# Kernel optimization log

Measured on AMD Instinct MI355X. Metric: run time of the kernel, lower is better.

## Reference

```python
import jax, jax.numpy as jnp
import numpy as np

BITW = 1
BITA = 3
BATCH = 8192
IN_CH = 4096
N_UNITS = 4096


def _quantize(x, k):
    # DoReFa uniform quantizer with straight-through estimator (round -> identity grad)
    n = float(2 ** k - 1)
    return x + jax.lax.stop_gradient(jnp.round(x * n) / n - x)


def _cabs(x):
    # clip magnitude to [0, 1]
    return jnp.minimum(1.0, jnp.abs(x))


def quantize_active(x, bitA):
    if bitA == 32:
        return x
    return _quantize(x, bitA)


def quantize_weight(w, bitW):
    if bitW == 32:
        return w
    if bitW == 1:
        # binary weights scaled by mean |w| (E is treated as constant)
        E = jax.lax.stop_gradient(jnp.mean(jnp.abs(w)))
        y = w / E
        # sign with straight-through gradient
        return (y + jax.lax.stop_gradient(jnp.sign(y) - y)) * E
    t = jnp.tanh(w)
    t = t / jnp.max(jnp.abs(t)) * 0.5 + 0.5
    return 2.0 * _quantize(t, bitW) - 1.0


def setup_inputs() -> dict:
    key = jax.random.key(0)
    k1, k2 = jax.random.split(key)
    inputs = jax.random.normal(k1, (BATCH, IN_CH), dtype=jnp.float32)
    # truncated_normal(stddev=0.1) init approximated with normal * 0.1
    W = jax.random.normal(k2, (IN_CH, N_UNITS), dtype=jnp.float32) * 0.1
    b = jnp.zeros((N_UNITS,), dtype=jnp.float32)
    return {"inputs": inputs, "W": W, "b": b}


def reference(inputs, W, b):
    q_in = quantize_active(_cabs(inputs), BITA)   # [B, IN] in {0..1} grid of 2^bitA-1 levels
    q_W = quantize_weight(W, BITW)                # [IN, OUT] binary (+-E)
    out = jnp.matmul(q_in, q_W) + b               # [B, OUT]
    return out
```

## Files before the change

### kernel.cpp

```cpp
#include <hip/hip_runtime.h>


static constexpr int BATCH  = 8192;
static constexpr int IN_CH  = 4096;
static constexpr int NUNITS = 4096;
static constexpr int TPB    = 256;

typedef int v4i __attribute__((ext_vector_type(4)));

static constexpr size_t A8_OFF   = 0;
static constexpr size_t A8_BYTES = (size_t)BATCH * IN_CH;
static constexpr size_t BT_OFF   = A8_OFF + A8_BYTES;
static constexpr size_t BT_BYTES = (size_t)NUNITS * IN_CH;
static constexpr int    NPART    = 4096;
static constexpr size_t PART_OFF = BT_OFF + BT_BYTES;
static constexpr size_t SCALE_OFF= PART_OFF + NPART * sizeof(float);

__global__ __launch_bounds__(TPB) void k_signT(const float* __restrict__ W,
                                               char* __restrict__ bt,
                                               float* __restrict__ partials) {
    __shared__ char tile[64][68];
    __shared__ float red[TPB];
    const int bk = blockIdx.x & 63;
    const int bn = blockIdx.x >> 6;
    const int t  = threadIdx.x;
    const int c4 = (t & 15) * 4;
    const int r0 = t >> 4;
    float asum = 0.f;
#pragma unroll
    for (int i = 0; i < 4; ++i) {
        const int r = i * 16 + r0;
        float4 w = *(const float4*)(W + (size_t)(bk * 64 + r) * NUNITS + bn * 64 + c4);
        asum += fabsf(w.x) + fabsf(w.y) + fabsf(w.z) + fabsf(w.w);
        tile[c4 + 0][r] = (w.x > 0.f) ? 1 : ((w.x < 0.f) ? -1 : 0);
        tile[c4 + 1][r] = (w.y > 0.f) ? 1 : ((w.y < 0.f) ? -1 : 0);
        tile[c4 + 2][r] = (w.z > 0.f) ? 1 : ((w.z < 0.f) ? -1 : 0);
        tile[c4 + 3][r] = (w.w > 0.f) ? 1 : ((w.w < 0.f) ? -1 : 0);
    }
    __syncthreads();
    const int n  = t >> 2;
    const int kk = (t & 3) * 16;
    char o[16];
#pragma unroll
    for (int j = 0; j < 16; ++j) o[j] = tile[n][kk + j];
    *(uint4*)(bt + (size_t)(bn * 64 + n) * IN_CH + bk * 64 + kk) = *(const uint4*)o;

    red[t] = asum;
    __syncthreads();
    for (int off = TPB / 2; off > 0; off >>= 1) {
        if (t < off) red[t] += red[t + off];
        __syncthreads();
    }
    if (t == 0) partials[blockIdx.x] = red[0];
}

__device__ __forceinline__ unsigned int q4(float4 v) {
    unsigned int b0 = (unsigned int)(int)rintf(fminf(1.0f, fabsf(v.x)) * 7.0f);
    unsigned int b1 = (unsigned int)(int)rintf(fminf(1.0f, fabsf(v.y)) * 7.0f);
    unsigned int b2 = (unsigned int)(int)rintf(fminf(1.0f, fabsf(v.z)) * 7.0f);
    unsigned int b3 = (unsigned int)(int)rintf(fminf(1.0f, fabsf(v.w)) * 7.0f);
    return b0 | (b1 << 8) | (b2 << 16) | (b3 << 24);
}

__global__ __launch_bounds__(TPB) void k_quant_a(const float4* __restrict__ x4,
                                                 uint4* __restrict__ a16,
                                                 const float* __restrict__ partials,
                                                 float* __restrict__ scale) {
    if (blockIdx.x == 0) {
        __shared__ float red[TPB];
        float s = 0.f;
        for (int i = threadIdx.x; i < NPART; i += TPB) s += partials[i];
        red[threadIdx.x] = s;
        __syncthreads();
        for (int off = TPB / 2; off > 0; off >>= 1) {
            if ((int)threadIdx.x < off) red[threadIdx.x] += red[threadIdx.x + off];
            __syncthreads();
        }
        if (threadIdx.x == 0) {
            float E = red[0] / (float)((size_t)IN_CH * NUNITS);
            *scale = E / 7.0f;
        }
    }
    const size_t t = (size_t)blockIdx.x * TPB + threadIdx.x;
    uint4 o;
    o.x = q4(x4[t * 4 + 0]);
    o.y = q4(x4[t * 4 + 1]);
    o.z = q4(x4[t * 4 + 2]);
    o.w = q4(x4[t * 4 + 3]);
    a16[t] = o;
}

__device__ __forceinline__ void gload_lds16(const void* g, void* l) {
    __builtin_amdgcn_global_load_lds((const __attribute__((address_space(1))) void*)g,
                                     (__attribute__((address_space(3))) void*)l,
                                     16, 0, 0);
}

#define VMCNT0   asm volatile("s_waitcnt vmcnt(0)" ::: "memory")
#define LGKM0    asm volatile("s_waitcnt lgkmcnt(0)" ::: "memory")
#define SCHEDB   __builtin_amdgcn_sched_barrier(0)
#define BARRIER  __builtin_amdgcn_s_barrier()
#define PRIO1    __builtin_amdgcn_s_setprio(1)
#define PRIO0    __builtin_amdgcn_s_setprio(0)

static constexpr int NI = IN_CH / 128;

__global__ __launch_bounds__(1024, 4) void k_gemm(const char* __restrict__ A8,
                                                  const char* __restrict__ BT,
                                                  const float* __restrict__ scale_p,
                                                  const float* __restrict__ bias,
                                                  float* __restrict__ out) {
    __shared__ char Ms[2][65536];

    const int t    = threadIdx.x;
    const int bid  = blockIdx.x;
    const int swzb = (bid & 7) * 64 + (bid >> 3);
    const int bRow = swzb >> 4;
    const int bCol = swzb & 15;
    const int lane = t & 63;
    const int wid  = t >> 6;
    const int wr   = wid >> 2;
    const int wc   = wid & 3;
    const int lr   = lane & 15;
    const int lk4  = lane >> 4;

    const int aoff = ((lk4 ^ (lr & 7)) << 4);
    const int boff = aoff ^ 64;

    const int lslot = (t & 7) ^ ((t >> 3) & 7);
    const char* mbase = (lslot < 4)
        ? (A8 + (size_t)(bRow * 256) * IN_CH)
        : (BT + (size_t)(bCol * 256) * IN_CH);
    const char* sbase = mbase + (size_t)(t >> 3) * IN_CH + ((lslot & 3) << 4);

    v4i acc[4][4] = {};

#define STAGE4(P, STG)                                                           \
    _Pragma("unroll") for (int c = 0; c < 2; ++c)                                \
        _Pragma("unroll") for (int h = 0; h < 2; ++h)                            \
            gload_lds16(sbase + (size_t)h * 128 * IN_CH + ((size_t)(P) * 128 + c * 64), \
                        (STG) + c * 32768 + h * 16384 + t * 16)

#define CHUNK(CUR, c)                                                            \
    do {                                                                         \
        const char* _cp = (CUR) + (c) * 32768;                                   \
        v4i a_[4], b_[4];                                                        \
        _Pragma("unroll") for (int m = 0; m < 4; ++m)                            \
            a_[m] = *(const v4i*)(_cp + (wr * 64 + m * 16 + lr) * 128 + aoff);   \
        _Pragma("unroll") for (int n = 0; n < 4; ++n)                            \
            b_[n] = *(const v4i*)(_cp + (wc * 64 + n * 16 + lr) * 128 + boff);   \
        PRIO1;                                                                   \
        _Pragma("unroll") for (int m = 0; m < 4; ++m)                            \
            _Pragma("unroll") for (int n = 0; n < 4; ++n)                        \
                acc[m][n] = __builtin_amdgcn_mfma_i32_16x16x64_i8(               \
                    a_[m], b_[n], acc[m][n], 0, 0, 0);                           \
        PRIO0;                                                                   \
    } while (0)

#define INTERVAL(P, CUR, STG, DOSTG)                                             \
    do {                                                                         \
        SCHEDB; LGKM0;                                                           \
        VMCNT0;                                                                  \
        BARRIER; SCHEDB;                                                         \
        if (DOSTG) { STAGE4((P) + 1, STG); }                                     \
        CHUNK(CUR, 0);                                                           \
        CHUNK(CUR, 1);                                                           \
    } while (0)

    char* B0 = (char*)Ms[0];
    char* B1 = (char*)Ms[1];

    STAGE4(0, B0);

    for (int P = 0; P < NI - 2; P += 2) {
        INTERVAL(P,     B0, B1, 1);
        INTERVAL(P + 1, B1, B0, 1);
    }
    INTERVAL(NI - 2, B0, B1, 1);
    INTERVAL(NI - 1, B1, B0, 0);

    const float scale = *scale_p;
    const int orow0 = bRow * 256 + wr * 64;
    const int ocol0 = bCol * 256 + wc * 64;
#pragma unroll
    for (int m = 0; m < 4; ++m) {
#pragma unroll
        for (int n = 0; n < 4; ++n) {
            const int col = ocol0 + n * 16 + lr;
            const float bb = bias[col];
            const int rbase = orow0 + m * 16 + lk4 * 4;
#pragma unroll
            for (int j = 0; j < 4; ++j)
                out[(size_t)(rbase + j) * NUNITS + col] = scale * (float)acc[m][n][j] + bb;
        }
    }
#undef STAGE4
#undef CHUNK
#undef INTERVAL
}

extern "C" void kernel_launch(void* const* d_in, const int* in_sizes, int n_in,
                              void* d_out, int out_size, void* d_ws, size_t ws_size,
                              hipStream_t stream) {
    const float* x  = (const float*)d_in[0];
    const float* W  = (const float*)d_in[1];
    const float* b  = (const float*)d_in[2];
    float* out      = (float*)d_out;

    char*  ws       = (char*)d_ws;
    char*  A8       = ws + A8_OFF;
    char*  BT       = ws + BT_OFF;
    float* partials = (float*)(ws + PART_OFF);
    float* scale    = (float*)(ws + SCALE_OFF);

    k_signT<<<(IN_CH / 64) * (NUNITS / 64), TPB, 0, stream>>>(W, BT, partials);
    k_quant_a<<<(BATCH * (IN_CH / 16)) / TPB, TPB, 0, stream>>>((const float4*)x, (uint4*)A8,
                                                                partials, scale);
    k_gemm<<<(BATCH / 256) * (NUNITS / 256), 1024, 0, stream>>>(A8, BT, scale, b, out);
}
```

Measured before the change: 167.6 us.

## Pack binary weights to 2 bits in MFMA fragment order and expand in-register

The sign kernel now writes weight signs as 2-bit codes packed into dwords, laid out in the exact per-lane fragment order the GEMM consumes. The GEMM stages only a quarter of the previous B bytes into LDS and expands each packed dword to int8 fragments with v_perm lookups before the MFMAs. The A tile layout and swizzle are reorganised to match the smaller LDS footprint. This cuts global and LDS traffic for B, but adds VALU permute work inside the MFMA loop, and the B staging now uses 4-byte direct-to-LDS loads.

Result: slower. 248.1 us (+48.0%).

```diff
diff --git a/kernel.cpp b/kernel.cpp
--- a/kernel.cpp
+++ b/kernel.cpp
@@ -10,14 +10,14 @@
 
 static constexpr size_t A8_OFF   = 0;
 static constexpr size_t A8_BYTES = (size_t)BATCH * IN_CH;
-static constexpr size_t BT_OFF   = A8_OFF + A8_BYTES;
-static constexpr size_t BT_BYTES = (size_t)NUNITS * IN_CH;
+static constexpr size_t PB_OFF   = A8_OFF + A8_BYTES;
+static constexpr size_t PB_BYTES = (size_t)NUNITS * IN_CH / 4;
 static constexpr int    NPART    = 4096;
-static constexpr size_t PART_OFF = BT_OFF + BT_BYTES;
+static constexpr size_t PART_OFF = PB_OFF + PB_BYTES;
 static constexpr size_t SCALE_OFF= PART_OFF + NPART * sizeof(float);
 
 __global__ __launch_bounds__(TPB) void k_signT(const float* __restrict__ W,
-                                               char* __restrict__ bt,
+                                               unsigned int* __restrict__ pb,
                                                float* __restrict__ partials) {
     __shared__ char tile[64][68];
     __shared__ float red[TPB];
@@ -38,12 +38,16 @@
         tile[c4 + 3][r] = (w.w > 0.f) ? 1 : ((w.w < 0.f) ? -1 : 0);
     }
     __syncthreads();
-    const int n  = t >> 2;
-    const int kk = (t & 3) * 16;
-    char o[16];
-#pragma unroll
-    for (int j = 0; j < 16; ++j) o[j] = tile[n][kk + j];
-    *(uint4*)(bt + (size_t)(bn * 64 + n) * IN_CH + bk * 64 + kk) = *(const uint4*)o;
+    const int cl   = t & 63;
+    const int lk4p = t >> 6;
+    unsigned int d = 0;
+#pragma unroll
+    for (int j = 0; j < 16; ++j)
+        d |= ((unsigned int)(unsigned char)tile[cl][lk4p * 16 + j] & 3u) << (2 * j);
+    const int lanep = lk4p * 16 + (cl & 15);
+    const size_t dw = (size_t)(bn >> 2) * 65536 + (size_t)bk * 1024
+                    + (size_t)(bn & 3) * 256 + lanep * 4 + (cl >> 4);
+    pb[dw] = d;
 
     red[t] = asum;
     __syncthreads();
@@ -95,6 +99,41 @@
                                      (__attribute__((address_space(3))) void*)l,
                                      16, 0, 0);
 }
+__device__ __forceinline__ void gload_lds4(const void* g, void* l) {
+    __builtin_amdgcn_global_load_lds((const __attribute__((address_space(1))) void*)g,
+                                     (__attribute__((address_space(3))) void*)l,
+                                     4, 0, 0);
+}
+
+__device__ __forceinline__ unsigned int vperm(unsigned int s0, unsigned int s1,
+                                              unsigned int sel) {
+    unsigned int d;
+    asm("v_perm_b32 %0, %1, %2, %3" : "=v"(d) : "v"(s0), "v"(s1), "v"(sel));
+    return d;
+}
+
+__device__ __forceinline__ v4i expand2b(unsigned int p, unsigned int lut) {
+    const unsigned int M = 0x03030303u;
+    unsigned int t0 = p & M;
+    unsigned int t1 = (p >> 2) & M;
+    unsigned int t2 = (p >> 4) & M;
+    unsigned int t3 = (p >> 6) & M;
+    t0 = vperm(lut, lut, t0);
+    t1 = vperm(lut, lut, t1);
+    t2 = vperm(lut, lut, t2);
+    t3 = vperm(lut, lut, t3);
+    v4i b;
+    unsigned int q, r;
+    q = vperm(t1, t0, 0x0C0C0400u); r = vperm(t3, t2, 0x0C0C0400u);
+    b[0] = (int)vperm(r, q, 0x05040100u);
+    q = vperm(t1, t0, 0x0C0C0501u); r = vperm(t3, t2, 0x0C0C0501u);
+    b[1] = (int)vperm(r, q, 0x05040100u);
+    q = vperm(t1, t0, 0x0C0C0602u); r = vperm(t3, t2, 0x0C0C0602u);
+    b[2] = (int)vperm(r, q, 0x05040100u);
+    q = vperm(t1, t0, 0x0C0C0703u); r = vperm(t3, t2, 0x0C0C0703u);
+    b[3] = (int)vperm(r, q, 0x05040100u);
+    return b;
+}
 
 #define VMCNT0   asm volatile("s_waitcnt vmcnt(0)" ::: "memory")
 #define LGKM0    asm volatile("s_waitcnt lgkmcnt(0)" ::: "memory")
@@ -106,11 +145,12 @@
 static constexpr int NI = IN_CH / 128;
 
 __global__ __launch_bounds__(1024, 4) void k_gemm(const char* __restrict__ A8,
-                                                  const char* __restrict__ BT,
+                                                  const unsigned int* __restrict__ PB,
                                                   const float* __restrict__ scale_p,
                                                   const float* __restrict__ bias,
                                                   float* __restrict__ out) {
-    __shared__ char Ms[2][65536];
+    __shared__ char As[2][32768];
+    __shared__ char Ps[2][8192];
 
     const int t    = threadIdx.x;
     const int bid  = blockIdx.x;
@@ -124,37 +164,53 @@
     const int lr   = lane & 15;
     const int lk4  = lane >> 4;
 
-    const int aoff = ((lk4 ^ (lr & 7)) << 4);
-    const int boff = aoff ^ 64;
-
-    const int lslot = (t & 7) ^ ((t >> 3) & 7);
-    const char* mbase = (lslot < 4)
-        ? (A8 + (size_t)(bRow * 256) * IN_CH)
-        : (BT + (size_t)(bCol * 256) * IN_CH);
-    const char* sbase = mbase + (size_t)(t >> 3) * IN_CH + ((lslot & 3) << 4);
+    int aoff0, aoff1, aoff2, aoff3;
+    {
+        const int r0_ = wr * 64 + 0 * 16 + lr, l0 = r0_ & 127;
+        const int r1_ = wr * 64 + 1 * 16 + lr, l1 = r1_ & 127;
+        const int r2_ = wr * 64 + 2 * 16 + lr, l2 = r2_ & 127;
+        const int r3_ = wr * 64 + 3 * 16 + lr, l3 = r3_ & 127;
+        aoff0 = l0 * 128 + (((((r0_ >> 7) << 2) | lk4) ^ (l0 & 7)) << 4);
+        aoff1 = l1 * 128 + (((((r1_ >> 7) << 2) | lk4) ^ (l1 & 7)) << 4);
+        aoff2 = l2 * 128 + (((((r2_ >> 7) << 2) | lk4) ^ (l2 & 7)) << 4);
+        aoff3 = l3 * 128 + (((((r3_ >> 7) << 2) | lk4) ^ (l3 & 7)) << 4);
+    }
+    const int pboff = wc * 1024 + lane * 16;
+
+    const int s_log   = (t & 7) ^ ((t >> 3) & 7);
+    const int rowbase = ((s_log >> 2) << 7) + (t >> 3);
+    const char* sA    = A8 + (size_t)(bRow * 256 + rowbase) * IN_CH + ((s_log & 3) << 4);
+    const unsigned int* pbg = PB + (size_t)bCol * 65536 + t;
+
+    const unsigned int lut = 0xFF000100u;
 
     v4i acc[4][4] = {};
 
-#define STAGE4(P, STG)                                                           \
-    _Pragma("unroll") for (int c = 0; c < 2; ++c)                                \
-        _Pragma("unroll") for (int h = 0; h < 2; ++h)                            \
-            gload_lds16(sbase + (size_t)h * 128 * IN_CH + ((size_t)(P) * 128 + c * 64), \
-                        (STG) + c * 32768 + h * 16384 + t * 16)
-
-#define CHUNK(CUR, c)                                                            \
+#define STAGE(P, BI)                                                             \
     do {                                                                         \
-        const char* _cp = (CUR) + (c) * 32768;                                   \
-        v4i a_[4], b_[4];                                                        \
-        _Pragma("unroll") for (int m = 0; m < 4; ++m)                            \
-            a_[m] = *(const v4i*)(_cp + (wr * 64 + m * 16 + lr) * 128 + aoff);   \
-        _Pragma("unroll") for (int n = 0; n < 4; ++n)                            \
-            b_[n] = *(const v4i*)(_cp + (wc * 64 + n * 16 + lr) * 128 + boff);   \
-        PRIO1;                                                                   \
-        _Pragma("unroll") for (int m = 0; m < 4; ++m)                            \
-            _Pragma("unroll") for (int n = 0; n < 4; ++n)                        \
-                acc[m][n] = __builtin_amdgcn_mfma_i32_16x16x64_i8(               \
-                    a_[m], b_[n], acc[m][n], 0, 0, 0);                           \
-        PRIO0;                                                                   \
+        gload_lds16(sA + (size_t)(P) * 128 +  0, &As[BI][0]     + t * 16);       \
+        gload_lds16(sA + (size_t)(P) * 128 + 64, &As[BI][16384] + t * 16);       \
+        gload_lds4(pbg + (size_t)(P) * 2048,        &Ps[BI][0]    + t * 4);      \
+        gload_lds4(pbg + (size_t)(P) * 2048 + 1024, &Ps[BI][4096] + t * 4);      \
+    } while (0)
+
+#define CHUNK(BI, c)                                                             \
+    do {                                                                         \
+        const char* _ap = &As[BI][(c) * 16384];                                  \
+        v4i a0 = *(const v4i*)(_ap + aoff0);                                     \
+        v4i a1 = *(const v4i*)(_ap + aoff1);                                     \
+        v4i a2 = *(const v4i*)(_ap + aoff2);                                     \
+        v4i a3 = *(const v4i*)(_ap + aoff3);                                     \
+        v4i bp = *(const v4i*)(&Ps[BI][(c) * 4096] + pboff);                     \
+        _Pragma("unroll") for (int n = 0; n < 4; ++n) {                          \
+            v4i b = expand2b((unsigned int)bp[n], lut);                          \
+            PRIO1;                                                               \
+            acc[0][n] = __builtin_amdgcn_mfma_i32_16x16x64_i8(a0, b, acc[0][n], 0, 0, 0); \
+            acc[1][n] = __builtin_amdgcn_mfma_i32_16x16x64_i8(a1, b, acc[1][n], 0, 0, 0); \
+            acc[2][n] = __builtin_amdgcn_mfma_i32_16x16x64_i8(a2, b, acc[2][n], 0, 0, 0); \
+            acc[3][n] = __builtin_amdgcn_mfma_i32_16x16x64_i8(a3, b, acc[3][n], 0, 0, 0); \
+            PRIO0;                                                               \
+        }                                                                        \
     } while (0)
 
 #define INTERVAL(P, CUR, STG, DOSTG)                                             \
@@ -162,22 +218,19 @@
         SCHEDB; LGKM0;                                                           \
         VMCNT0;                                                                  \
         BARRIER; SCHEDB;                                                         \
-        if (DOSTG) { STAGE4((P) + 1, STG); }                                     \
+        if (DOSTG) { STAGE((P) + 1, STG); }                                      \
         CHUNK(CUR, 0);                                                           \
         CHUNK(CUR, 1);                                                           \
     } while (0)
 
-    char* B0 = (char*)Ms[0];
-    char* B1 = (char*)Ms[1];
-
-    STAGE4(0, B0);
+    STAGE(0, 0);
 
     for (int P = 0; P < NI - 2; P += 2) {
-        INTERVAL(P,     B0, B1, 1);
-        INTERVAL(P + 1, B1, B0, 1);
-    }
-    INTERVAL(NI - 2, B0, B1, 1);
-    INTERVAL(NI - 1, B1, B0, 0);
+        INTERVAL(P,     0, 1, 1);
+        INTERVAL(P + 1, 1, 0, 1);
+    }
+    INTERVAL(NI - 2, 0, 1, 1);
+    INTERVAL(NI - 1, 1, 0, 0);
 
     const float scale = *scale_p;
     const int orow0 = bRow * 256 + wr * 64;
@@ -194,7 +247,7 @@
                 out[(size_t)(rbase + j) * NUNITS + col] = scale * (float)acc[m][n][j] + bb;
         }
     }
-#undef STAGE4
+#undef STAGE
 #undef CHUNK
 #undef INTERVAL
 }
@@ -209,12 +262,12 @@
 
     char*  ws       = (char*)d_ws;
     char*  A8       = ws + A8_OFF;
-    char*  BT       = ws + BT_OFF;
+    unsigned int* PB = (unsigned int*)(ws + PB_OFF);
     float* partials = (float*)(ws + PART_OFF);
     float* scale    = (float*)(ws + SCALE_OFF);
 
-    k_signT<<<(IN_CH / 64) * (NUNITS / 64), TPB, 0, stream>>>(W, BT, partials);
+    k_signT<<<(IN_CH / 64) * (NUNITS / 64), TPB, 0, stream>>>(W, PB, partials);
     k_quant_a<<<(BATCH * (IN_CH / 16)) / TPB, TPB, 0, stream>>>((const float4*)x, (uint4*)A8,
                                                                 partials, scale);
-    k_gemm<<<(BATCH / 256) * (NUNITS / 256), 1024, 0, stream>>>(A8, BT, scale, b, out);
-}
+    k_gemm<<<(BATCH / 256) * (NUNITS / 256), 1024, 0, stream>>>(A8, PB, scale, b, out);
+}
```
